# Optimization experiments

Hardware: AMD Instinct MI355X
Metric: run time of the kernel (lower is better)

Reference implementation:

```python
import jax, jax.numpy as jnp
import numpy as np


def setup_inputs() -> dict:
    key = jax.random.key(0)
    k1, k2, k3 = jax.random.split(key, 3)
    n_way, n_shot, d, n_query = 5, 10, 1024, 16384
    n_support = n_way * n_shot
    train_imgs = jax.random.normal(k1, (n_support, d), dtype=jnp.float32)
    # one-hot labels: exactly n_shot examples per class (interleaved)
    cls = jnp.tile(jnp.arange(n_way), n_shot)  # [n_support]
    train_labels = jax.nn.one_hot(cls, n_way, dtype=jnp.int64)
    query_imgs = jax.random.normal(k2, (n_query, d), dtype=jnp.float32)
    query_labels = jax.random.randint(k3, (n_query,), 0, n_way)
    return {"train_imgs": train_imgs, "train_labels": train_labels,
            "query_imgs": query_imgs, "query_labels": query_labels}


def reference(train_imgs, train_labels, query_imgs, query_labels):
    # backbone = identity: imgs are already feature embeddings
    n_support, n_way = train_labels.shape
    n_shot = n_support // n_way  # static
    support = train_imgs                      # [n_support, d]
    query = query_imgs                        # [n_query, d]

    # group support features by class: [n_way, n_shot, d]
    cls = jnp.argmax(train_labels, axis=1)
    order = jnp.argsort(cls, stable=True)
    grouped = support[order].reshape(n_way, n_shot, -1)
    mats = jnp.swapaxes(grouped, 1, 2)        # [n_way, d, n_shot]

    # batched reduced SVD (torch.svd some=True -> full_matrices=False)
    U, _, _ = jnp.linalg.svd(mats, full_matrices=False)  # [n_way, d, n_shot]
    Uk = U[:, :, : n_shot - 1]                # [n_way, d, k]

    # projection of queries onto each class subspace: P = Uk Uk^T q
    coeff = jnp.einsum('wdk,qd->wkq', Uk, query)   # [n_way, k, n_query]
    proj = jnp.einsum('wdk,wkq->wqd', Uk, coeff)   # [n_way, n_query, d]
    dist = jnp.sum((query[None, :, :] - proj) ** 2, axis=-1)  # [n_way, n_query]

    logits = -dist.T                           # [n_query, n_way]
    # normalize=False in this configuration
    return jax.nn.log_softmax(logits, axis=1)
```

## Files before the change

### kernel.cpp

```cpp
#include <hip/hip_runtime.h>
#include <stdint.h>


typedef __attribute__((ext_vector_type(4))) float f32x4;
typedef __attribute__((ext_vector_type(8))) short s16x8;

#define WS_G_OFF    0
#define WS_GH_OFF   4096
#define WS_P_OFF    8192
#define WS_Z_OFF    262144

#define RDL(x, l) __uint_as_float(__builtin_amdgcn_readlane(__float_as_uint(x), (l)))

__device__ __forceinline__ unsigned short f2bf(float f) {
  unsigned int u = __float_as_uint(f);
  u += 0x7FFFu + ((u >> 16) & 1u);
  return (unsigned short)(u >> 16);
}

__device__ __forceinline__ bool labels_int64(const int* L) {
  int cnt = 0; bool oddz = true;
  #pragma unroll
  for (int t = 0; t < 20; ++t) {
    int v = L[t];
    if (t & 1) { if (v) oddz = false; }
    else       { if (v) cnt++; }
  }
  return oddz && (cnt == 2);
}

__device__ __forceinline__ int cls_of(const int* L, bool is64, int i) {
  int best = -0x7fffffff, c = 0;
  #pragma unroll
  for (int j = 0; j < 5; ++j) {
    int v = is64 ? L[i * 10 + 2 * j] : L[i * 5 + j];
    if (v > best) { best = v; c = j; }
  }
  return c;
}

__global__ __launch_bounds__(256) void dsn_prep(const float* __restrict__ support,
                                                const int* __restrict__ labels,
                                                double* __restrict__ G,
                                                unsigned short* __restrict__ P) {
  int b = blockIdx.x;
  bool is64 = labels_int64(labels);

  if (b < 69) {
    int wid  = b * 4 + (threadIdx.x >> 6);
    int lane = threadIdx.x & 63;
    if (wid >= 275) return;
    int w = wid / 55, p = wid % 55;
    int a = 0;
    while (p >= 10 - a) { p -= 10 - a; a++; }
    int bb = a + p;

    int myc = (lane < 50) ? cls_of(labels, is64, lane) : -1;
    unsigned long long mask = __ballot(lane < 50 && myc == w);

    unsigned long long m = mask;
    for (int i = 0; i < a; ++i) m &= m - 1;
    int ia = __ffsll((unsigned long long)m) - 1;
    m = mask;
    for (int i = 0; i < bb; ++i) m &= m - 1;
    int ib = __ffsll((unsigned long long)m) - 1;

    const float* A = support + ia * 1024;
    const float* B = support + ib * 1024;
    double acc = 0.0;
    #pragma unroll
    for (int i = 0; i < 16; ++i) {
      int d = lane + 64 * i;
      acc += (double)A[d] * (double)B[d];
    }
    #pragma unroll
    for (int off = 32; off > 0; off >>= 1) acc += __shfl_xor(acc, off);
    if (lane == 0) {
      G[(w * 10 + a) * 10 + bb] = acc;
      G[(w * 10 + bb) * 10 + a] = acc;
    }
  } else {
    int r = b - 69;
    int w = r >> 4, kk = r & 15;
    int t = threadIdx.x;
    unsigned short* Prow = P + r * 1024;
    if (kk >= 10) {
      #pragma unroll
      for (int j = 0; j < 4; ++j) Prow[t + 256 * j] = 0;
      return;
    }
    __shared__ int sid;
    if (t < 64) {
      int myc = (t < 50) ? cls_of(labels, is64, t) : -1;
      unsigned long long mask = __ballot(t < 50 && myc == w);
      if (t == 0) {
        unsigned long long m = mask;
        for (int z = 0; z < kk; ++z) m &= m - 1;
        sid = __ffsll(m) - 1;
      }
    }
    __syncthreads();
    const float* src = support + (size_t)sid * 1024;
    #pragma unroll
    for (int j = 0; j < 4; ++j) Prow[t + 256 * j] = f2bf(src[t + 256 * j]);
  }
}

__global__ __launch_bounds__(256, 4) void dsn_zs(const float* __restrict__ query,
                                                 const unsigned short* __restrict__ P,
                                                 const double* __restrict__ G,
                                                 float* __restrict__ Ghat,
                                                 float* __restrict__ Z) {
  if (blockIdx.x < 5) {
    if (threadIdx.x >= 64) return;
    int w = blockIdx.x;
    int li = threadIdx.x;
    int rr = (li < 10) ? li : 0;
    const double* Gr = G + w * 100 + rr * 10;

    float o[10], g[10], h[10];
    #pragma unroll
    for (int j = 0; j < 10; ++j) {
      o[j] = (float)Gr[j];
      g[j] = o[j];
      h[j] = (li == j) ? 1.f : 0.f;
    }

    #pragma unroll
    for (int k = 0; k < 10; ++k) {
      float piv = 1.f / RDL(g[k], k);
      float pg[10], ph[10];
      #pragma unroll
      for (int j = 0; j < 10; ++j) {
        pg[j] = RDL(g[j], k) * piv;
        ph[j] = RDL(h[j], k) * piv;
      }
      float f = g[k];
      bool isk = (li == k);
      #pragma unroll
      for (int j = 0; j < 10; ++j) {
        g[j] = isk ? pg[j] : g[j] - f * pg[j];
        h[j] = isk ? ph[j] : h[j] - f * ph[j];
      }
    }

    float b[10];
    float d = h[0];
    #pragma unroll
    for (int k = 1; k < 10; ++k) d = (li == k) ? h[k] : d;
    float dm = RDL(d, 0);
    #pragma unroll
    for (int k = 1; k < 10; ++k) dm = fmaxf(dm, RDL(d, k));
    float rn = 1.f / dm;
    #pragma unroll
    for (int j = 0; j < 10; ++j) b[j] = h[j] * rn;
    float db = d * rn;

    int jmx = 0;
    float bv = RDL(db, 0);
    float trB = bv;
    #pragma unroll
    for (int k = 1; k < 10; ++k) {
      float t2 = RDL(db, k);
      trB += t2;
      if (t2 > bv) { bv = t2; jmx = k; }
    }
    float sigma = (trB - bv) * (1.f / 9.f);
    sigma = fminf(fmaxf(sigma, 0.f), 0.92f);
    float rs = 1.f / (bv - sigma);

    float x = (li == jmx) ? 1.f : 0.f;
    #pragma unroll
    for (int it = 0; it < 16; ++it) {
      float xn = 0.f;
      #pragma unroll
      for (int k = 0; k < 10; ++k) xn += b[k] * RDL(x, k);
      x = rs * (xn - sigma * x);
    }
    #pragma unroll
    for (int it = 0; it < 2; ++it) {
      float xn = 0.f;
      #pragma unroll
      for (int k = 0; k < 10; ++k) xn += b[k] * RDL(x, k);
      float ax = fabsf(xn);
      float mx = RDL(ax, 0);
      #pragma unroll
      for (int k = 1; k < 10; ++k) mx = fmaxf(mx, RDL(ax, k));
      x = xn * (1.f / mx);
    }
    float v = x;

    float gv = 0.f;
    #pragma unroll
    for (int k = 0; k < 10; ++k) gv += o[k] * RDL(v, k);
    float tn = v * gv;
    float denom = RDL(tn, 0);
    #pragma unroll
    for (int k = 1; k < 10; ++k) denom += RDL(tn, k);
    float rden = 1.f / denom;
    if (li < 10) {
      #pragma unroll
      for (int j = 0; j < 10; ++j)
        Ghat[w * 100 + li * 10 + j] = h[j] - v * RDL(v, j) * rden;
    }
    return;
  }

  __shared__ float Zsh[4][80][17];

  int t    = threadIdx.x;
  int wave = t >> 6;
  int lane = t & 63;
  int q0   = (blockIdx.x - 5) * 16;
  int qrow = lane & 15;
  int kbase = wave * 256 + (lane >> 4) * 8;

  const float* qp = query + (size_t)(q0 + qrow) * 1024 + kbase;
  const unsigned short* up = P + qrow * 1024 + kbase;

  f32x4 acc[5];
  #pragma unroll
  for (int w = 0; w < 5; ++w) acc[w] = (f32x4){0.f, 0.f, 0.f, 0.f};

  #pragma unroll
  for (int kt = 0; kt < 8; ++kt) {
    const float* qk = qp + kt * 32;
    f32x4 lo = *(const f32x4*)qk;
    f32x4 hi = *(const f32x4*)(qk + 4);
    s16x8 bf;
    bf[0] = (short)f2bf(lo[0]); bf[1] = (short)f2bf(lo[1]);
    bf[2] = (short)f2bf(lo[2]); bf[3] = (short)f2bf(lo[3]);
    bf[4] = (short)f2bf(hi[0]); bf[5] = (short)f2bf(hi[1]);
    bf[6] = (short)f2bf(hi[2]); bf[7] = (short)f2bf(hi[3]);
    const unsigned short* uk = up + kt * 32;
    #pragma unroll
    for (int w = 0; w < 5; ++w) {
      s16x8 av = *(const s16x8*)(uk + w * 16384);
      acc[w] = __builtin_amdgcn_mfma_f32_16x16x32_bf16(av, bf, acc[w], 0, 0, 0);
    }
  }

  int rowbase = (lane >> 4) * 4;
  #pragma unroll
  for (int w = 0; w < 5; ++w) {
    #pragma unroll
    for (int r = 0; r < 4; ++r)
      Zsh[wave][w * 16 + rowbase + r][qrow] = acc[w][r];
  }
  __syncthreads();

  #pragma unroll
  for (int idx = 0; idx < 5; ++idx) {
    int e = t + idx * 256;
    int s = e >> 4, c = e & 15;
    float z = Zsh[0][s][c] + Zsh[1][s][c] + Zsh[2][s][c] + Zsh[3][s][c];
    Z[(size_t)s * 16384 + q0 + c] = z;
  }
}

__global__ __launch_bounds__(256) void dsn_post(const float* __restrict__ Ghat,
                                                const float* __restrict__ Z,
                                                float* __restrict__ out) {
  __shared__ float Gh[500];
  int t = threadIdx.x;
  for (int i = t; i < 500; i += 256) Gh[i] = Ghat[i];
  __syncthreads();
  int q = blockIdx.x * 256 + t;

  float zv[50];
  #pragma unroll
  for (int w = 0; w < 5; ++w)
    #pragma unroll
    for (int s = 0; s < 10; ++s)
      zv[w * 10 + s] = Z[(size_t)(w * 16 + s) * 16384 + q];

  float sv[5];
  #pragma unroll
  for (int w = 0; w < 5; ++w) {
    float s = 0.f;
    #pragma unroll
    for (int i = 0; i < 10; ++i) {
      float gz = 0.f;
      #pragma unroll
      for (int j = 0; j < 10; ++j) gz += Gh[w * 100 + i * 10 + j] * zv[w * 10 + j];
      s += zv[w * 10 + i] * gz;
    }
    sv[w] = s;
  }
  float mx = fmaxf(fmaxf(fmaxf(sv[0], sv[1]), fmaxf(sv[2], sv[3])), sv[4]);
  float sum = 0.f;
  #pragma unroll
  for (int w = 0; w < 5; ++w) sum += expf(sv[w] - mx);
  float lse = mx + logf(sum);
  float* o = out + (size_t)q * 5;
  #pragma unroll
  for (int w = 0; w < 5; ++w) o[w] = sv[w] - lse;
}

extern "C" void kernel_launch(void* const* d_in, const int* in_sizes, int n_in,
                              void* d_out, int out_size, void* d_ws, size_t ws_size,
                              hipStream_t stream) {
  const float* support = (const float*)d_in[0];
  const int*   labels  = (const int*)d_in[1];
  const float* query   = (const float*)d_in[2];
  float* out = (float*)d_out;
  char* ws = (char*)d_ws;

  double*         G    = (double*)(ws + WS_G_OFF);
  float*          Ghat = (float*)(ws + WS_GH_OFF);
  unsigned short* P    = (unsigned short*)(ws + WS_P_OFF);
  float*          Z    = (float*)(ws + WS_Z_OFF);

  int nq = in_sizes[2] / 1024;
  int zs_blocks = nq / 16 + 5;
  int post_blocks = nq / 256;

  hipLaunchKernelGGL(dsn_prep, dim3(149), dim3(256), 0, stream, support, labels, G, P);
  hipLaunchKernelGGL(dsn_zs,   dim3(zs_blocks), dim3(256), 0, stream,
                     query, P, G, Ghat, Z);
  hipLaunchKernelGGL(dsn_post, dim3(post_blocks), dim3(256), 0, stream, Ghat, Z, out);
}
```

Before: 42.92 us.

## Fuse Z projection with quadratic-form epilogue and split out Gram solve kernel

The small Gram-matrix inverse and eigen solve moves into its own 5-block kernel. The projection GEMM kernel then finishes each query's quadratic form and log-softmax from shared memory, so the Z intermediate no longer goes to global memory and is not read back by a separate post kernel. This removes the Z round trip through HBM, at the cost of an extra tiny serialized launch and an epilogue run by only 16 threads per block.

```diff
diff --git a/kernel.cpp b/kernel.cpp
--- a/kernel.cpp
+++ b/kernel.cpp
@@ -8,7 +8,6 @@
 #define WS_G_OFF    0
 #define WS_GH_OFF   4096
 #define WS_P_OFF    8192
-#define WS_Z_OFF    262144
 
 #define RDL(x, l) __uint_as_float(__builtin_amdgcn_readlane(__float_as_uint(x), (l)))
 
@@ -106,114 +105,118 @@
   }
 }
 
-__global__ __launch_bounds__(256, 4) void dsn_zs(const float* __restrict__ query,
-                                                 const unsigned short* __restrict__ P,
-                                                 const double* __restrict__ G,
-                                                 float* __restrict__ Ghat,
-                                                 float* __restrict__ Z) {
-  if (blockIdx.x < 5) {
-    if (threadIdx.x >= 64) return;
-    int w = blockIdx.x;
-    int li = threadIdx.x;
-    int rr = (li < 10) ? li : 0;
-    const double* Gr = G + w * 100 + rr * 10;
-
-    float o[10], g[10], h[10];
+__global__ __launch_bounds__(64) void dsn_solve(const double* __restrict__ G,
+                                                float* __restrict__ Ghat) {
+  int w = blockIdx.x;
+  int li = threadIdx.x;
+  int rr = (li < 10) ? li : 0;
+  const double* Gr = G + w * 100 + rr * 10;
+
+  float o[10], g[10], h[10];
+  #pragma unroll
+  for (int j = 0; j < 10; ++j) {
+    o[j] = (float)Gr[j];
+    g[j] = o[j];
+    h[j] = (li == j) ? 1.f : 0.f;
+  }
+
+  #pragma unroll
+  for (int k = 0; k < 10; ++k) {
+    float piv = 1.f / RDL(g[k], k);
+    float pg[10], ph[10];
     #pragma unroll
     for (int j = 0; j < 10; ++j) {
-      o[j] = (float)Gr[j];
-      g[j] = o[j];
-      h[j] = (li == j) ? 1.f : 0.f;
-    }
-
-    #pragma unroll
-    for (int k = 0; k < 10; ++k) {
-      float piv = 1.f / RDL(g[k], k);
-      float pg[10], ph[10];
-      #pragma unroll
-      for (int j = 0; j < 10; ++j) {
-        pg[j] = RDL(g[j], k) * piv;
-        ph[j] = RDL(h[j], k) * piv;
-      }
-      float f = g[k];
-      bool isk = (li == k);
-      #pragma unroll
-      for (int j = 0; j < 10; ++j) {
-        g[j] = isk ? pg[j] : g[j] - f * pg[j];
-        h[j] = isk ? ph[j] : h[j] - f * ph[j];
-      }
-    }
-
-    float b[10];
-    float d = h[0];
-    #pragma unroll
-    for (int k = 1; k < 10; ++k) d = (li == k) ? h[k] : d;
-    float dm = RDL(d, 0);
-    #pragma unroll
-    for (int k = 1; k < 10; ++k) dm = fmaxf(dm, RDL(d, k));
-    float rn = 1.f / dm;
-    #pragma unroll
-    for (int j = 0; j < 10; ++j) b[j] = h[j] * rn;
-    float db = d * rn;
-
-    int jmx = 0;
-    float bv = RDL(db, 0);
-    float trB = bv;
-    #pragma unroll
-    for (int k = 1; k < 10; ++k) {
-      float t2 = RDL(db, k);
-      trB += t2;
-      if (t2 > bv) { bv = t2; jmx = k; }
-    }
-    float sigma = (trB - bv) * (1.f / 9.f);
-    sigma = fminf(fmaxf(sigma, 0.f), 0.92f);
-    float rs = 1.f / (bv - sigma);
-
-    float x = (li == jmx) ? 1.f : 0.f;
-    #pragma unroll
-    for (int it = 0; it < 16; ++it) {
-      float xn = 0.f;
-      #pragma unroll
-      for (int k = 0; k < 10; ++k) xn += b[k] * RDL(x, k);
-      x = rs * (xn - sigma * x);
-    }
-    #pragma unroll
-    for (int it = 0; it < 2; ++it) {
-      float xn = 0.f;
-      #pragma unroll
-      for (int k = 0; k < 10; ++k) xn += b[k] * RDL(x, k);
-      float ax = fabsf(xn);
-      float mx = RDL(ax, 0);
-      #pragma unroll
-      for (int k = 1; k < 10; ++k) mx = fmaxf(mx, RDL(ax, k));
-      x = xn * (1.f / mx);
-    }
-    float v = x;
-
-    float gv = 0.f;
-    #pragma unroll
-    for (int k = 0; k < 10; ++k) gv += o[k] * RDL(v, k);
-    float tn = v * gv;
-    float denom = RDL(tn, 0);
-    #pragma unroll
-    for (int k = 1; k < 10; ++k) denom += RDL(tn, k);
-    float rden = 1.f / denom;
-    if (li < 10) {
-      #pragma unroll
-      for (int j = 0; j < 10; ++j)
-        Ghat[w * 100 + li * 10 + j] = h[j] - v * RDL(v, j) * rden;
-    }
-    return;
-  }
-
+      pg[j] = RDL(g[j], k) * piv;
+      ph[j] = RDL(h[j], k) * piv;
+    }
+    float f = g[k];
+    bool isk = (li == k);
+    #pragma unroll
+    for (int j = 0; j < 10; ++j) {
+      g[j] = isk ? pg[j] : g[j] - f * pg[j];
+      h[j] = isk ? ph[j] : h[j] - f * ph[j];
+    }
+  }
+
+  float b[10];
+  float d = h[0];
+  #pragma unroll
+  for (int k = 1; k < 10; ++k) d = (li == k) ? h[k] : d;
+  float dm = RDL(d, 0);
+  #pragma unroll
+  for (int k = 1; k < 10; ++k) dm = fmaxf(dm, RDL(d, k));
+  float rn = 1.f / dm;
+  #pragma unroll
+  for (int j = 0; j < 10; ++j) b[j] = h[j] * rn;
+  float db = d * rn;
+
+  int jmx = 0;
+  float bv = RDL(db, 0);
+  float trB = bv;
+  #pragma unroll
+  for (int k = 1; k < 10; ++k) {
+    float t2 = RDL(db, k);
+    trB += t2;
+    if (t2 > bv) { bv = t2; jmx = k; }
+  }
+  float sigma = (trB - bv) * (1.f / 9.f);
+  sigma = fminf(fmaxf(sigma, 0.f), 0.92f);
+  float rs = 1.f / (bv - sigma);
+
+  float x = (li == jmx) ? 1.f : 0.f;
+  #pragma unroll
+  for (int it = 0; it < 16; ++it) {
+    float xn = 0.f;
+    #pragma unroll
+    for (int k = 0; k < 10; ++k) xn += b[k] * RDL(x, k);
+    x = rs * (xn - sigma * x);
+  }
+  #pragma unroll
+  for (int it = 0; it < 2; ++it) {
+    float xn = 0.f;
+    #pragma unroll
+    for (int k = 0; k < 10; ++k) xn += b[k] * RDL(x, k);
+    float ax = fabsf(xn);
+    float mx = RDL(ax, 0);
+    #pragma unroll
+    for (int k = 1; k < 10; ++k) mx = fmaxf(mx, RDL(ax, k));
+    x = xn * (1.f / mx);
+  }
+  float v = x;
+
+  float gv = 0.f;
+  #pragma unroll
+  for (int k = 0; k < 10; ++k) gv += o[k] * RDL(v, k);
+  float tn = v * gv;
+  float denom = RDL(tn, 0);
+  #pragma unroll
+  for (int k = 1; k < 10; ++k) denom += RDL(tn, k);
+  float rden = 1.f / denom;
+  if (li < 10) {
+    #pragma unroll
+    for (int j = 0; j < 10; ++j)
+      Ghat[w * 100 + li * 10 + j] = h[j] - v * RDL(v, j) * rden;
+  }
+}
+
+__global__ __launch_bounds__(256, 4) void dsn_main(const float* __restrict__ query,
+                                                   const unsigned short* __restrict__ P,
+                                                   const float* __restrict__ Ghat,
+                                                   float* __restrict__ out) {
   __shared__ float Zsh[4][80][17];
+  __shared__ float Ghs[500];
 
   int t    = threadIdx.x;
   int wave = t >> 6;
   int lane = t & 63;
-  int q0   = (blockIdx.x - 5) * 16;
+  int q0   = blockIdx.x * 16;
   int qrow = lane & 15;
   int kbase = wave * 256 + (lane >> 4) * 8;
+
+  if (t < 250) {
+    Ghs[t]       = Ghat[t];
+    Ghs[t + 250] = Ghat[t + 250];
+  }
 
   const float* qp = query + (size_t)(q0 + qrow) * 1024 + kbase;
   const unsigned short* up = P + qrow * 1024 + kbase;
@@ -249,52 +252,41 @@
   }
   __syncthreads();
 
-  #pragma unroll
-  for (int idx = 0; idx < 5; ++idx) {
-    int e = t + idx * 256;
-    int s = e >> 4, c = e & 15;
-    float z = Zsh[0][s][c] + Zsh[1][s][c] + Zsh[2][s][c] + Zsh[3][s][c];
-    Z[(size_t)s * 16384 + q0 + c] = z;
-  }
-}
-
-__global__ __launch_bounds__(256) void dsn_post(const float* __restrict__ Ghat,
-                                                const float* __restrict__ Z,
-                                                float* __restrict__ out) {
-  __shared__ float Gh[500];
-  int t = threadIdx.x;
-  for (int i = t; i < 500; i += 256) Gh[i] = Ghat[i];
-  __syncthreads();
-  int q = blockIdx.x * 256 + t;
-
-  float zv[50];
-  #pragma unroll
-  for (int w = 0; w < 5; ++w)
-    #pragma unroll
-    for (int s = 0; s < 10; ++s)
-      zv[w * 10 + s] = Z[(size_t)(w * 16 + s) * 16384 + q];
-
-  float sv[5];
-  #pragma unroll
-  for (int w = 0; w < 5; ++w) {
-    float s = 0.f;
-    #pragma unroll
-    for (int i = 0; i < 10; ++i) {
-      float gz = 0.f;
+  if (t < 16) {
+    int q = q0 + t;
+    float zv[50];
+    #pragma unroll
+    for (int w = 0; w < 5; ++w) {
       #pragma unroll
-      for (int j = 0; j < 10; ++j) gz += Gh[w * 100 + i * 10 + j] * zv[w * 10 + j];
-      s += zv[w * 10 + i] * gz;
-    }
-    sv[w] = s;
-  }
-  float mx = fmaxf(fmaxf(fmaxf(sv[0], sv[1]), fmaxf(sv[2], sv[3])), sv[4]);
-  float sum = 0.f;
-  #pragma unroll
-  for (int w = 0; w < 5; ++w) sum += expf(sv[w] - mx);
-  float lse = mx + logf(sum);
-  float* o = out + (size_t)q * 5;
-  #pragma unroll
-  for (int w = 0; w < 5; ++w) o[w] = sv[w] - lse;
+      for (int s = 0; s < 10; ++s) {
+        float z = Zsh[0][w * 16 + s][t];
+        #pragma unroll
+        for (int sp = 1; sp < 4; ++sp) z += Zsh[sp][w * 16 + s][t];
+        zv[w * 10 + s] = z;
+      }
+    }
+    float sv[5];
+    #pragma unroll
+    for (int w = 0; w < 5; ++w) {
+      float s = 0.f;
+      #pragma unroll
+      for (int i = 0; i < 10; ++i) {
+        float gz = 0.f;
+        #pragma unroll
+        for (int j = 0; j < 10; ++j) gz += Ghs[w * 100 + i * 10 + j] * zv[w * 10 + j];
+        s += zv[w * 10 + i] * gz;
+      }
+      sv[w] = s;
+    }
+    float mx = fmaxf(fmaxf(fmaxf(sv[0], sv[1]), fmaxf(sv[2], sv[3])), sv[4]);
+    float sum = 0.f;
+    #pragma unroll
+    for (int w = 0; w < 5; ++w) sum += expf(sv[w] - mx);
+    float lse = mx + logf(sum);
+    float* o = out + (size_t)q * 5;
+    #pragma unroll
+    for (int w = 0; w < 5; ++w) o[w] = sv[w] - lse;
+  }
 }
 
 extern "C" void kernel_launch(void* const* d_in, const int* in_sizes, int n_in,
@@ -309,14 +301,12 @@
   double*         G    = (double*)(ws + WS_G_OFF);
   float*          Ghat = (float*)(ws + WS_GH_OFF);
   unsigned short* P    = (unsigned short*)(ws + WS_P_OFF);
-  float*          Z    = (float*)(ws + WS_Z_OFF);
 
   int nq = in_sizes[2] / 1024;
-  int zs_blocks = nq / 16 + 5;
-  int post_blocks = nq / 256;
-
-  hipLaunchKernelGGL(dsn_prep, dim3(149), dim3(256), 0, stream, support, labels, G, P);
-  hipLaunchKernelGGL(dsn_zs,   dim3(zs_blocks), dim3(256), 0, stream,
-                     query, P, G, Ghat, Z);
-  hipLaunchKernelGGL(dsn_post, dim3(post_blocks), dim3(256), 0, stream, Ghat, Z, out);
-}
+  int main_blocks = nq / 16;
+
+  hipLaunchKernelGGL(dsn_prep,  dim3(149), dim3(256), 0, stream, support, labels, G, P);
+  hipLaunchKernelGGL(dsn_solve, dim3(5),   dim3(64),  0, stream, G, Ghat);
+  hipLaunchKernelGGL(dsn_main,  dim3(main_blocks), dim3(256), 0, stream,
+                     query, P, Ghat, out);
+}
```

Result: slower. 47.51 us (+10.7%).
